# Optimization experiments

Measured on AMD Instinct MI355X. Metric: run time of the kernel, lower is better.

## Reference

```python
import jax, jax.numpy as jnp
import numpy as np
from functools import partial

NUM_HEADS = 6

def _l2norm(x, axis=-1, eps=1e-12):
    n = jnp.sqrt(jnp.sum(x * x, axis=axis, keepdims=True))
    return x / jnp.maximum(n, eps)

def setup_inputs() -> dict:
    key = jax.random.key(0)
    ks = jax.random.split(key, 6)
    b, c, h, w = 2, 192, 256, 256
    x = jax.random.normal(ks[0], (b, c, h, w), dtype=jnp.float32)
    qkv_w = jax.random.normal(ks[1], (3 * c, c), dtype=jnp.float32) * (1.0 / np.sqrt(c))
    dw_w = jax.random.normal(ks[2], (3 * c, 1, 3, 3), dtype=jnp.float32) * (1.0 / 3.0)
    proj_w = jax.random.normal(ks[3], (c, c), dtype=jnp.float32) * (1.0 / np.sqrt(c))
    temperature = jnp.ones((NUM_HEADS, 1, 1), dtype=jnp.float32)
    attn1 = jnp.full((1,), 0.2, dtype=jnp.float32)
    return {"x": x, "qkv_w": qkv_w, "dw_w": dw_w, "proj_w": proj_w,
            "temperature": temperature, "attn1": attn1}

def reference(x, qkv_w, dw_w, proj_w, temperature, attn1):
    b, c, h, w = x.shape
    heads = NUM_HEADS
    C = c // heads          # per-head channel count; attention length
    N = h * w               # spatial 'feature' dim
    # 1x1 conv dim -> 3*dim
    qkv = jnp.einsum('bchw,oc->bohw', x, qkv_w)
    # 3x3 depthwise conv over all 3*dim channels (groups = 3*dim)
    qkv = jax.lax.conv_general_dilated(
        qkv, dw_w, window_strides=(1, 1), padding='SAME',
        feature_group_count=3 * c,
        dimension_numbers=('NCHW', 'OIHW', 'NCHW'))
    q, k, v = jnp.split(qkv, 3, axis=1)
    # b (head C) h w -> b head C (h w)
    q = q.reshape(b, heads, C, N)
    k = k.reshape(b, heads, C, N)
    v = v.reshape(b, heads, C, N)
    q = _l2norm(q)
    k = _l2norm(k)
    # channel attention: [b, head, C, C], tiny matrix
    attn = jnp.einsum('bhcn,bhdn->bhcd', q, k) * temperature[None]
    # top-k (k = C//2) selective mask; kth value threshold == scatter mask
    k1 = C // 2
    kth = jax.lax.top_k(attn, k1)[0][..., -1:]
    attn_m = jnp.where(attn >= kth, attn, -jnp.inf)
    a1 = jax.nn.softmax(attn_m, axis=-1)
    out = jnp.einsum('bhcd,bhdn->bhcn', a1, v)
    # NOTE: original code also computes 2/3, 3/4, 4/5 top-k branches but the
    # returned output uses only out1 * self.attn1 (others are dead code).
    out = out * attn1[0]
    out = out.reshape(b, c, h, w)
    out = jnp.einsum('bchw,oc->bohw', out, proj_w)
    return out
```

## Files before the change

### kernel.cpp

```cpp
#include <hip/hip_runtime.h>
#include <math.h>

#define N_SP 65536
#define IMG  256

typedef __attribute__((ext_vector_type(8))) short s16x8;
typedef __attribute__((ext_vector_type(4))) float f32x4;

__device__ inline ushort f2bf(float f) {
    uint u = __float_as_uint(f);
    return (ushort)((u + 0x7FFFu + ((u >> 16) & 1u)) >> 16);
}
__device__ inline float bf2f(ushort h) { return __uint_as_float(((uint)h) << 16); }
__device__ inline uint pk2(ushort a, ushort b) { return (uint)a | ((uint)b << 16); }

__device__ __forceinline__ void load_lds16(const ushort* g, ushort* l) {
    __builtin_amdgcn_global_load_lds(
        (const __attribute__((address_space(1))) void*)g,
        (__attribute__((address_space(3))) void*)l, 16, 0, 0);
}

__global__ __launch_bounds__(256) void transp_conv(
    const float* __restrict__ src, ushort* __restrict__ hi, ushort* __restrict__ lo)
{
    __shared__ float T[32][65];
    const int t = threadIdx.x;
    const int n0 = blockIdx.x * 64, c0 = blockIdx.y * 32;
    {
        const int cb = t >> 6, n = t & 63;
        #pragma unroll
        for (int i = 0; i < 8; ++i) {
            const int c = cb + i * 4;
            T[c][n] = src[(long long)(c0 + c) * N_SP + n0 + n];
        }
    }
    __syncthreads();
    const int n = t >> 2, cq = (t & 3) * 8;
    float v[8];
    #pragma unroll
    for (int j = 0; j < 8; ++j) v[j] = T[cq + j][n];
    ushort h[8], l[8];
    #pragma unroll
    for (int j = 0; j < 8; ++j) { h[j] = f2bf(v[j]); l[j] = f2bf(v[j] - bf2f(h[j])); }
    uint4 H, L;
    H.x = pk2(h[0], h[1]); H.y = pk2(h[2], h[3]); H.z = pk2(h[4], h[5]); H.w = pk2(h[6], h[7]);
    L.x = pk2(l[0], l[1]); L.y = pk2(l[2], l[3]); L.z = pk2(l[4], l[5]); L.w = pk2(l[6], l[7]);
    const long long o = (long long)(n0 + n) * 192 + c0 + cq;
    *(uint4*)(hi + o) = H;
    *(uint4*)(lo + o) = L;
}

__global__ __launch_bounds__(256) void gemm_mfma(
    const float* __restrict__ Wf, int wrow0,
    const ushort* __restrict__ XtHi, const ushort* __restrict__ XtLo,
    float* __restrict__ C)
{
    __shared__ ushort WsH[64][40], WsL[64][40];
    __shared__ ushort XsH[256 * 32], XsL[256 * 32];
    const int t  = threadIdx.x;
    const int wv = t >> 6, l = t & 63;
    const int lc = l & 15, lg = l >> 4;
    const int m0 = blockIdx.y * 64;
    const long long n0 = (long long)blockIdx.x * 256;

    f32x4 acc[4][4];
    #pragma unroll
    for (int i = 0; i < 4; ++i)
        #pragma unroll
        for (int j = 0; j < 4; ++j) acc[i][j] = (f32x4)(0.f);

    const int ar = t >> 2, ak = (t & 3) * 8;
    const int rX  = wv * 64 + (l >> 2);
    const int koX = (l & 3) * 8;
    ushort* lH = &XsH[(wv * 64) * 32];
    ushort* lL = &XsL[(wv * 64) * 32];

    for (int kc = 0; kc < 192; kc += 32) {
        {
            const ushort* gH = XtHi + (n0 + rX) * 192 + kc + koX;
            const ushort* gL = XtLo + (n0 + rX) * 192 + kc + koX;
            #pragma unroll
            for (int i = 0; i < 4; ++i) {
                load_lds16(gH + i * (16 * 192), lH + i * (16 * 32));
                load_lds16(gL + i * (16 * 192), lL + i * (16 * 32));
            }
        }
        {
            const float* wp = Wf + (long long)(wrow0 + m0 + ar) * 192 + kc + ak;
            const float4 a0 = *(const float4*)wp;
            const float4 a1 = *(const float4*)(wp + 4);
            const float v[8] = {a0.x, a0.y, a0.z, a0.w, a1.x, a1.y, a1.z, a1.w};
            ushort h[8], lo_[8];
            #pragma unroll
            for (int j = 0; j < 8; ++j) { h[j] = f2bf(v[j]); lo_[j] = f2bf(v[j] - bf2f(h[j])); }
            uint4 H, L;
            H.x = pk2(h[0],h[1]); H.y = pk2(h[2],h[3]); H.z = pk2(h[4],h[5]); H.w = pk2(h[6],h[7]);
            L.x = pk2(lo_[0],lo_[1]); L.y = pk2(lo_[2],lo_[3]); L.z = pk2(lo_[4],lo_[5]); L.w = pk2(lo_[6],lo_[7]);
            *(uint4*)&WsH[ar][ak] = H;
            *(uint4*)&WsL[ar][ak] = L;
        }
        __syncthreads();

        s16x8 ah[4], al[4];
        #pragma unroll
        for (int mf = 0; mf < 4; ++mf) {
            ah[mf] = *(const s16x8*)&WsH[mf * 16 + lc][lg * 8];
            al[mf] = *(const s16x8*)&WsL[mf * 16 + lc][lg * 8];
        }
        #pragma unroll
        for (int nf = 0; nf < 4; ++nf) {
            const int nr = wv * 64 + nf * 16 + lc;
            const s16x8 bh = *(const s16x8*)&XsH[nr * 32 + lg * 8];
            const s16x8 bl = *(const s16x8*)&XsL[nr * 32 + lg * 8];
            #pragma unroll
            for (int mf = 0; mf < 4; ++mf) {
                acc[mf][nf] = __builtin_amdgcn_mfma_f32_16x16x32_bf16(ah[mf], bh, acc[mf][nf], 0, 0, 0);
                acc[mf][nf] = __builtin_amdgcn_mfma_f32_16x16x32_bf16(ah[mf], bl, acc[mf][nf], 0, 0, 0);
                acc[mf][nf] = __builtin_amdgcn_mfma_f32_16x16x32_bf16(al[mf], bh, acc[mf][nf], 0, 0, 0);
            }
        }
        __syncthreads();
    }

    #pragma unroll
    for (int mf = 0; mf < 4; ++mf)
        #pragma unroll
        for (int nf = 0; nf < 4; ++nf) {
            const long long nn = n0 + wv * 64 + nf * 16 + lc;
            #pragma unroll
            for (int j = 0; j < 4; ++j)
                C[(long long)(m0 + mf * 16 + lg * 4 + j) * N_SP + nn] = acc[mf][nf][j];
        }
}

__global__ __launch_bounds__(256) void dwconv8(
    const float* __restrict__ src, const float* __restrict__ dww, float* __restrict__ dst)
{
    const int t = threadIdx.x;
    const int s = blockIdx.x * 256 + t;
    const int y = s >> 5;
    const int x8 = (s & 31) * 8;
    const int cg = blockIdx.y;

    const int xl = (x8 == 0) ? 0 : x8 - 4;
    const int xr = (x8 == 248) ? 248 : x8 + 8;

    #pragma unroll
    for (int i = 0; i < 4; ++i) {
        const int c = cg * 4 + i;
        const float* base = src + ((long long)c << 16);
        const float* wp = dww + c * 9;
        float acc[8];
        #pragma unroll
        for (int j = 0; j < 8; ++j) acc[j] = 0.f;
        #pragma unroll
        for (int dy = 0; dy < 3; ++dy) {
            const int yy = y + dy - 1;
            const bool vld = (yy >= 0 && yy < IMG);
            const float* row = base + (vld ? yy : y) * IMG;
            const float w0 = vld ? wp[dy * 3 + 0] : 0.f;
            const float w1 = vld ? wp[dy * 3 + 1] : 0.f;
            const float w2 = vld ? wp[dy * 3 + 2] : 0.f;
            const float4 Lq = *(const float4*)(row + xl);
            const float4 M0 = *(const float4*)(row + x8);
            const float4 M1 = *(const float4*)(row + x8 + 4);
            const float4 Rq = *(const float4*)(row + xr);
            float vv[10];
            vv[0] = (x8 == 0) ? 0.f : Lq.w;
            vv[1] = M0.x; vv[2] = M0.y; vv[3] = M0.z; vv[4] = M0.w;
            vv[5] = M1.x; vv[6] = M1.y; vv[7] = M1.z; vv[8] = M1.w;
            vv[9] = (x8 == 248) ? 0.f : Rq.x;
            #pragma unroll
            for (int j = 0; j < 8; ++j)
                acc[j] = fmaf(w0, vv[j], fmaf(w1, vv[j + 1], fmaf(w2, vv[j + 2], acc[j])));
        }
        float4 o0, o1;
        o0.x = acc[0]; o0.y = acc[1]; o0.z = acc[2]; o0.w = acc[3];
        o1.x = acc[4]; o1.y = acc[5]; o1.z = acc[6]; o1.w = acc[7];
        float* drow = dst + ((long long)c << 16) + y * IMG + x8;
        *(float4*)drow = o0;
        *(float4*)(drow + 4) = o1;
    }
}

__global__ __launch_bounds__(256) void dwconv_vt(
    const float* __restrict__ src, const float* __restrict__ dww,
    ushort* __restrict__ hi, ushort* __restrict__ lo)
{
    const int t = threadIdx.x;
    const int y  = blockIdx.x;
    const int cg = blockIdx.y;
    const int pxg = t & 31, chq = t >> 5;
    const int x8 = pxg * 8;
    const int c0 = cg * 32 + chq * 4;

    const int xl = (x8 == 0) ? 0 : x8 - 4;
    const int xr = (x8 == 248) ? 248 : x8 + 8;

    float accA[4][8];
    #pragma unroll
    for (int i = 0; i < 4; ++i) {
        const int c = c0 + i;
        const float* base = src + ((long long)c << 16);
        const float* wp = dww + c * 9;
        #pragma unroll
        for (int j = 0; j < 8; ++j) accA[i][j] = 0.f;
        #pragma unroll
        for (int dy = 0; dy < 3; ++dy) {
            const int yy = y + dy - 1;
            const bool vld = (yy >= 0 && yy < IMG);
            const float* row = base + (vld ? yy : y) * IMG;
            const float w0 = vld ? wp[dy * 3 + 0] : 0.f;
            const float w1 = vld ? wp[dy * 3 + 1] : 0.f;
            const float w2 = vld ? wp[dy * 3 + 2] : 0.f;
            const float4 Lq = *(const float4*)(row + xl);
            const float4 M0 = *(const float4*)(row + x8);
            const float4 M1 = *(const float4*)(row + x8 + 4);
            const float4 Rq = *(const float4*)(row + xr);
            float vv[10];
            vv[0] = (x8 == 0) ? 0.f : Lq.w;
            vv[1] = M0.x; vv[2] = M0.y; vv[3] = M0.z; vv[4] = M0.w;
            vv[5] = M1.x; vv[6] = M1.y; vv[7] = M1.z; vv[8] = M1.w;
            vv[9] = (x8 == 248) ? 0.f : Rq.x;
            #pragma unroll
            for (int j = 0; j < 8; ++j)
                accA[i][j] = fmaf(w0, vv[j], fmaf(w1, vv[j + 1], fmaf(w2, vv[j + 2], accA[i][j])));
        }
    }
    const long long nbase = (long long)y * 256 + x8;
    #pragma unroll
    for (int j = 0; j < 8; ++j) {
        ushort h4[4], l4[4];
        #pragma unroll
        for (int i = 0; i < 4; ++i) {
            const float v = accA[i][j];
            h4[i] = f2bf(v);
            l4[i] = f2bf(v - bf2f(h4[i]));
        }
        uint2 H, L;
        H.x = pk2(h4[0], h4[1]); H.y = pk2(h4[2], h4[3]);
        L.x = pk2(l4[0], l4[1]); L.y = pk2(l4[2], l4[3]);
        const long long o = (nbase + j) * 192 + c0;
        *(uint2*)(hi + o) = H;
        *(uint2*)(lo + o) = L;
    }
}

__global__ __launch_bounds__(256) void gred(
    const float* __restrict__ q, const float* __restrict__ k, float* __restrict__ Gpart)
{
    __shared__ float smem[8448];
    float* qs = smem;
    float* ks = smem + 4224;
    const int t = threadIdx.x;
    const int blk = blockIdx.x, h = blockIdx.y;
    const int w = t >> 6, l = t & 63;
    const int cqd = l >> 3, dqd = l & 7;

    float acc[4][4];
    #pragma unroll
    for (int i = 0; i < 4; ++i) { acc[i][0]=0.f; acc[i][1]=0.f; acc[i][2]=0.f; acc[i][3]=0.f; }
    float sq[4] = {0.f,0.f,0.f,0.f}, sk[4] = {0.f,0.f,0.f,0.f};

    const float* qh = q + ((long long)(h * 32) << 16);
    const float* kh = k + ((long long)(h * 32) << 16);

    for (int s = 0; s < 4; ++s) {
        const int n0s = blk * 512 + s * 128;
        #pragma unroll
        for (int i = 0; i < 4; ++i) {
            const int f4 = t + i * 256;
            const int ch = f4 >> 5, n4 = (f4 & 31) * 4;
            const long long go = ((long long)ch << 16) + n0s + n4;
            *(float4*)&qs[ch * 132 + n4] = *(const float4*)(qh + go);
            *(float4*)&ks[ch * 132 + n4] = *(const float4*)(kh + go);
        }
        __syncthreads();
        const int nb = w * 32;
        #pragma unroll
        for (int it = 0; it < 8; ++it) {
            const int n = nb + it * 4;
            float4 qa[4], kb[4];
            #pragma unroll
            for (int i = 0; i < 4; ++i) qa[i] = *(const float4*)&qs[(cqd * 4 + i) * 132 + n];
            #pragma unroll
            for (int j = 0; j < 4; ++j) kb[j] = *(const float4*)&ks[(dqd * 4 + j) * 132 + n];
            #pragma unroll
            for (int i = 0; i < 4; ++i) {
                #pragma unroll
                for (int j = 0; j < 4; ++j) {
                    acc[i][j] = fmaf(qa[i].x, kb[j].x, acc[i][j]);
                    acc[i][j] = fmaf(qa[i].y, kb[j].y, acc[i][j]);
                    acc[i][j] = fmaf(qa[i].z, kb[j].z, acc[i][j]);
                    acc[i][j] = fmaf(qa[i].w, kb[j].w, acc[i][j]);
                }
            }
            if (dqd == 0) {
                #pragma unroll
                for (int i = 0; i < 4; ++i) {
                    sq[i] = fmaf(qa[i].x, qa[i].x, sq[i]);
                    sq[i] = fmaf(qa[i].y, qa[i].y, sq[i]);
                    sq[i] = fmaf(qa[i].z, qa[i].z, sq[i]);
                    sq[i] = fmaf(qa[i].w, qa[i].w, sq[i]);
                }
            }
            if (cqd == 0) {
                #pragma unroll
                for (int j = 0; j < 4; ++j) {
                    sk[j] = fmaf(kb[j].x, kb[j].x, sk[j]);
                    sk[j] = fmaf(kb[j].y, kb[j].y, sk[j]);
                    sk[j] = fmaf(kb[j].z, kb[j].z, sk[j]);
                    sk[j] = fmaf(kb[j].w, kb[j].w, sk[j]);
                }
            }
        }
        __syncthreads();
    }

    float* red  = smem;
    float* red2 = smem + 4096;
    #pragma unroll
    for (int i = 0; i < 4; ++i) {
        #pragma unroll
        for (int j = 0; j < 4; ++j)
            red[w * 1024 + (cqd * 4 + i) * 32 + dqd * 4 + j] = acc[i][j];
    }
    if (dqd == 0) {
        #pragma unroll
        for (int i = 0; i < 4; ++i) red2[w * 32 + cqd * 4 + i] = sq[i];
    }
    if (cqd == 0) {
        #pragma unroll
        for (int j = 0; j < 4; ++j) red2[128 + w * 32 + dqd * 4 + j] = sk[j];
    }
    __syncthreads();

    float* Gp = Gpart + (long long)(h * 128 + blk) * 1088;
    #pragma unroll
    for (int i = 0; i < 4; ++i) {
        int slot = t + i * 256;
        Gp[slot] = red[slot] + red[1024 + slot] + red[2048 + slot] + red[3072 + slot];
    }
    if (t < 32) {
        Gp[1024 + t] = red2[t] + red2[32 + t] + red2[64 + t] + red2[96 + t];
    } else if (t < 64) {
        int c = t - 32;
        Gp[1056 + c] = red2[128 + c] + red2[160 + c] + red2[192 + c] + red2[224 + c];
    }
}

__global__ void reduce_g(const float* __restrict__ Gpart, float* __restrict__ G,
                         float* __restrict__ Sq, float* __restrict__ Sk, int bh0)
{
    const int h = blockIdx.x, t = threadIdx.x;
    const float* Gp = Gpart + (long long)h * 128 * 1088;
    const int bh = bh0 + h;
    #pragma unroll
    for (int i = 0; i < 5; ++i) {
        int slot = t + i * 256;
        if (slot >= 1088) break;
        float s = 0.f;
        for (int tl = 0; tl < 128; ++tl) s += Gp[(long long)tl * 1088 + slot];
        if (slot < 1024)      G[(long long)bh * 1024 + slot] = s;
        else if (slot < 1056) Sq[bh * 32 + (slot - 1024)] = s;
        else                  Sk[bh * 32 + (slot - 1056)] = s;
    }
}

__global__ void attn_small(const float* __restrict__ G, const float* __restrict__ Sq,
                           const float* __restrict__ Sk, const float* __restrict__ temp,
                           const float* __restrict__ attn1, float* __restrict__ A)
{
    const int h = blockIdx.x, b = blockIdx.y, c = threadIdx.x;
    const int bh = b * 6 + h;
    const float* g = G + ((long long)bh * 32 + c) * 32;
    const float nq = fmaxf(sqrtf(Sq[bh * 32 + c]), 1e-12f);
    const float T  = temp[h];
    const float a1 = attn1[0];

    float a[32];
    #pragma unroll
    for (int d = 0; d < 32; ++d) {
        float nk = fmaxf(sqrtf(Sk[bh * 32 + d]), 1e-12f);
        a[d] = g[d] / (nq * nk) * T;
    }
    unsigned mask = 0u;
    float m = 0.f, kth = 0.f;
    for (int it = 0; it < 16; ++it) {
        float best = -3.4e38f; int bi = 0;
        #pragma unroll
        for (int d = 0; d < 32; ++d) {
            bool avail = ((mask >> d) & 1u) == 0u;
            if (avail && a[d] > best) { best = a[d]; bi = d; }
        }
        mask |= (1u << bi);
        if (it == 0) m = best;
        kth = best;
    }
    float denom = 0.f;
    #pragma unroll
    for (int d = 0; d < 32; ++d) if (a[d] >= kth) denom += expf(a[d] - m);
    const float inv = a1 / denom;
    float* Ar = A + ((long long)bh * 32 + c) * 32;
    #pragma unroll
    for (int d = 0; d < 32; ++d) Ar[d] = (a[d] >= kth) ? expf(a[d] - m) * inv : 0.f;
}

__global__ void make_m(const float* __restrict__ proj_w, const float* __restrict__ A,
                       float* __restrict__ M)
{
    const int o = blockIdx.x, b = blockIdx.y, j = threadIdx.x;
    const int hd = j >> 5, d = j & 31;
    const float* pw = proj_w + o * 192 + hd * 32;
    const float* Ah = A + ((long long)(b * 6 + hd) * 32) * 32 + d;
    float s = 0.f;
    #pragma unroll
    for (int cq = 0; cq < 32; ++cq) s = fmaf(pw[cq], Ah[cq * 32], s);
    M[((long long)(b * 192 + o)) * 192 + j] = s;
}

extern "C" void kernel_launch(void* const* d_in, const int* in_sizes, int n_in,
                              void* d_out, int out_size, void* d_ws, size_t ws_size,
                              hipStream_t stream)
{
    const float* x      = (const float*)d_in[0];
    const float* qkv_w  = (const float*)d_in[1];
    const float* dww    = (const float*)d_in[2];
    const float* proj_w = (const float*)d_in[3];
    const float* temp   = (const float*)d_in[4];
    const float* attn1  = (const float*)d_in[5];
    float* out = (float*)d_out;
    float* wsf = (float*)d_ws;

    float* G   = wsf;
    float* Sq  = G + 12288;
    float* Sk  = Sq + 384;
    float* A   = Sk + 384;
    float* Mm  = A + 12288;
    float* buf = Mm + 73728;

    const long long PL = 12582912LL;
    float* W1 = buf;
    float* W2 = buf + PL;
    float* R1 = out;
    float* R2 = out + PL;

    ushort* R1H = (ushort*)R1; ushort* R1L = R1H + PL;
    ushort* W1H = (ushort*)W1; ushort* W1L = W1H + PL;

    transp_conv<<<dim3(1024, 6), 256, 0, stream>>>(x, R1H, R1L);
    gemm_mfma<<<dim3(256, 6), 256, 0, stream>>>(qkv_w, 0, R1H, R1L, buf);
    dwconv8<<<dim3(32, 48), 256, 0, stream>>>(W1, dww, R2);
    dwconv8<<<dim3(32, 48), 256, 0, stream>>>(W2, dww + 192 * 9, W1);
    gred<<<dim3(128, 6), 256, 0, stream>>>(R2, W1, W2);
    reduce_g<<<dim3(6, 1), 256, 0, stream>>>(W2, G, Sq, Sk, 0);

    transp_conv<<<dim3(1024, 6), 256, 0, stream>>>(x + PL, R1H, R1L);
    gemm_mfma<<<dim3(256, 6), 256, 0, stream>>>(qkv_w, 0, R1H, R1L, buf);
    dwconv8<<<dim3(32, 48), 256, 0, stream>>>(W1, dww, R2);
    dwconv8<<<dim3(32, 48), 256, 0, stream>>>(W2, dww + 192 * 9, W1);
    gred<<<dim3(128, 6), 256, 0, stream>>>(R2, W1, W2);
    reduce_g<<<dim3(6, 1), 256, 0, stream>>>(W2, G, Sq, Sk, 6);

    attn_small<<<dim3(6, 2), 32, 0, stream>>>(G, Sq, Sk, temp, attn1, A);
    make_m<<<dim3(192, 2), 192, 0, stream>>>(proj_w, A, Mm);

    gemm_mfma<<<dim3(256, 3), 256, 0, stream>>>(qkv_w, 384, R1H, R1L, W2);
    dwconv_vt<<<dim3(256, 6), 256, 0, stream>>>(W2, dww + 384 * 9, W1H, W1L);
    gemm_mfma<<<dim3(256, 3), 256, 0, stream>>>(Mm + 36864, 0, W1H, W1L, R2);

    transp_conv<<<dim3(1024, 6), 256, 0, stream>>>(x, R1H, R1L);
    gemm_mfma<<<dim3(256, 3), 256, 0, stream>>>(qkv_w, 384, R1H, R1L, W2);
    dwconv_vt<<<dim3(256, 6), 256, 0, stream>>>(W2, dww + 384 * 9, W1H, W1L);
    gemm_mfma<<<dim3(256, 3), 256, 0, stream>>>(Mm, 0, W1H, W1L, R1);
}
```

Before: 656.0 us.

## Double-buffer LDS tiles in MFMA GEMM to overlap loads with compute

Restructures the 1x1-conv GEMM k-loop with double-buffered LDS for both weight and activation tiles. The next k-chunk's global-to-LDS loads and weight fetch are issued before the MFMA work on the current chunk, and it waits only afterwards. This cuts one barrier per iteration and hides load latency. In exchange it doubles LDS use, which may lower occupancy, and it drops the padding on the weight tile rows, which may add bank conflicts.

```diff
diff --git a/kernel.cpp b/kernel.cpp
--- a/kernel.cpp
+++ b/kernel.cpp
@@ -55,8 +55,8 @@
     const ushort* __restrict__ XtHi, const ushort* __restrict__ XtLo,
     float* __restrict__ C)
 {
-    __shared__ ushort WsH[64][40], WsL[64][40];
-    __shared__ ushort XsH[256 * 32], XsL[256 * 32];
+    __shared__ ushort WsH[2][2048], WsL[2][2048];
+    __shared__ ushort XsH[2][8192], XsL[2][8192];
     const int t  = threadIdx.x;
     const int wv = t >> 6, l = t & 63;
     const int lc = l & 15, lg = l >> 4;
@@ -72,54 +72,94 @@
     const int ar = t >> 2, ak = (t & 3) * 8;
     const int rX  = wv * 64 + (l >> 2);
     const int koX = (l & 3) * 8;
-    ushort* lH = &XsH[(wv * 64) * 32];
-    ushort* lL = &XsL[(wv * 64) * 32];
-
-    for (int kc = 0; kc < 192; kc += 32) {
+    const float*  wbase = Wf + (long long)(wrow0 + m0 + ar) * 192 + ak;
+    const ushort* gHb = XtHi + (n0 + rX) * 192 + koX;
+    const ushort* gLb = XtLo + (n0 + rX) * 192 + koX;
+
+    float4 wa, wb;
+
+    wa = *(const float4*)(wbase);
+    wb = *(const float4*)(wbase + 4);
+    {
+        ushort* lH = &XsH[0][(wv * 64) * 32];
+        ushort* lL = &XsL[0][(wv * 64) * 32];
+        #pragma unroll
+        for (int i = 0; i < 4; ++i) {
+            load_lds16(gHb + i * (16 * 192), lH + i * (16 * 32));
+            load_lds16(gLb + i * (16 * 192), lL + i * (16 * 32));
+        }
+    }
+    asm volatile("s_waitcnt vmcnt(0)" ::: "memory");
+    {
+        const float v0=wa.x,v1=wa.y,v2=wa.z,v3=wa.w,v4=wb.x,v5=wb.y,v6=wb.z,v7=wb.w;
+        ushort h0=f2bf(v0),h1=f2bf(v1),h2=f2bf(v2),h3=f2bf(v3),
+               h4=f2bf(v4),h5=f2bf(v5),h6=f2bf(v6),h7=f2bf(v7);
+        uint4 H, L;
+        H.x=pk2(h0,h1); H.y=pk2(h2,h3); H.z=pk2(h4,h5); H.w=pk2(h6,h7);
+        L.x=pk2(f2bf(v0-bf2f(h0)),f2bf(v1-bf2f(h1)));
+        L.y=pk2(f2bf(v2-bf2f(h2)),f2bf(v3-bf2f(h3)));
+        L.z=pk2(f2bf(v4-bf2f(h4)),f2bf(v5-bf2f(h5)));
+        L.w=pk2(f2bf(v6-bf2f(h6)),f2bf(v7-bf2f(h7)));
+        *(uint4*)&WsH[0][ar * 32 + ak] = H;
+        *(uint4*)&WsL[0][ar * 32 + ak] = L;
+    }
+    __syncthreads();
+
+    #pragma unroll
+    for (int ks = 0; ks < 6; ++ks) {
+        const int cur = ks & 1, nxt = cur ^ 1;
+        if (ks < 5) {
+            const int kc = (ks + 1) * 32;
+            wa = *(const float4*)(wbase + kc);
+            wb = *(const float4*)(wbase + kc + 4);
+            ushort* lH = &XsH[nxt][(wv * 64) * 32];
+            ushort* lL = &XsL[nxt][(wv * 64) * 32];
+            #pragma unroll
+            for (int i = 0; i < 4; ++i) {
+                load_lds16(gHb + kc + i * (16 * 192), lH + i * (16 * 32));
+                load_lds16(gLb + kc + i * (16 * 192), lL + i * (16 * 32));
+            }
+            __builtin_amdgcn_sched_barrier(0);
+        }
         {
-            const ushort* gH = XtHi + (n0 + rX) * 192 + kc + koX;
-            const ushort* gL = XtLo + (n0 + rX) * 192 + kc + koX;
-            #pragma unroll
-            for (int i = 0; i < 4; ++i) {
-                load_lds16(gH + i * (16 * 192), lH + i * (16 * 32));
-                load_lds16(gL + i * (16 * 192), lL + i * (16 * 32));
-            }
-        }
-        {
-            const float* wp = Wf + (long long)(wrow0 + m0 + ar) * 192 + kc + ak;
-            const float4 a0 = *(const float4*)wp;
-            const float4 a1 = *(const float4*)(wp + 4);
-            const float v[8] = {a0.x, a0.y, a0.z, a0.w, a1.x, a1.y, a1.z, a1.w};
-            ushort h[8], lo_[8];
-            #pragma unroll
-            for (int j = 0; j < 8; ++j) { h[j] = f2bf(v[j]); lo_[j] = f2bf(v[j] - bf2f(h[j])); }
-            uint4 H, L;
-            H.x = pk2(h[0],h[1]); H.y = pk2(h[2],h[3]); H.z = pk2(h[4],h[5]); H.w = pk2(h[6],h[7]);
-            L.x = pk2(lo_[0],lo_[1]); L.y = pk2(lo_[2],lo_[3]); L.z = pk2(lo_[4],lo_[5]); L.w = pk2(lo_[6],lo_[7]);
-            *(uint4*)&WsH[ar][ak] = H;
-            *(uint4*)&WsL[ar][ak] = L;
-        }
-        __syncthreads();
-
-        s16x8 ah[4], al[4];
-        #pragma unroll
-        for (int mf = 0; mf < 4; ++mf) {
-            ah[mf] = *(const s16x8*)&WsH[mf * 16 + lc][lg * 8];
-            al[mf] = *(const s16x8*)&WsL[mf * 16 + lc][lg * 8];
-        }
-        #pragma unroll
-        for (int nf = 0; nf < 4; ++nf) {
-            const int nr = wv * 64 + nf * 16 + lc;
-            const s16x8 bh = *(const s16x8*)&XsH[nr * 32 + lg * 8];
-            const s16x8 bl = *(const s16x8*)&XsL[nr * 32 + lg * 8];
+            s16x8 ah[4], al[4];
             #pragma unroll
             for (int mf = 0; mf < 4; ++mf) {
-                acc[mf][nf] = __builtin_amdgcn_mfma_f32_16x16x32_bf16(ah[mf], bh, acc[mf][nf], 0, 0, 0);
-                acc[mf][nf] = __builtin_amdgcn_mfma_f32_16x16x32_bf16(ah[mf], bl, acc[mf][nf], 0, 0, 0);
-                acc[mf][nf] = __builtin_amdgcn_mfma_f32_16x16x32_bf16(al[mf], bh, acc[mf][nf], 0, 0, 0);
-            }
-        }
-        __syncthreads();
+                ah[mf] = *(const s16x8*)&WsH[cur][(mf * 16 + lc) * 32 + lg * 8];
+                al[mf] = *(const s16x8*)&WsL[cur][(mf * 16 + lc) * 32 + lg * 8];
+            }
+            #pragma unroll
+            for (int nf = 0; nf < 4; ++nf) {
+                const int nr = wv * 64 + nf * 16 + lc;
+                const s16x8 bh = *(const s16x8*)&XsH[cur][nr * 32 + lg * 8];
+                const s16x8 bl = *(const s16x8*)&XsL[cur][nr * 32 + lg * 8];
+                #pragma unroll
+                for (int mf = 0; mf < 4; ++mf) {
+                    acc[mf][nf] = __builtin_amdgcn_mfma_f32_16x16x32_bf16(ah[mf], bh, acc[mf][nf], 0, 0, 0);
+                    acc[mf][nf] = __builtin_amdgcn_mfma_f32_16x16x32_bf16(ah[mf], bl, acc[mf][nf], 0, 0, 0);
+                    acc[mf][nf] = __builtin_amdgcn_mfma_f32_16x16x32_bf16(al[mf], bh, acc[mf][nf], 0, 0, 0);
+                }
+            }
+        }
+        if (ks < 5) {
+            asm volatile("s_waitcnt vmcnt(0)" ::: "memory");
+            {
+                const float v0=wa.x,v1=wa.y,v2=wa.z,v3=wa.w,v4=wb.x,v5=wb.y,v6=wb.z,v7=wb.w;
+                ushort h0=f2bf(v0),h1=f2bf(v1),h2=f2bf(v2),h3=f2bf(v3),
+                       h4=f2bf(v4),h5=f2bf(v5),h6=f2bf(v6),h7=f2bf(v7);
+                uint4 H, L;
+                H.x=pk2(h0,h1); H.y=pk2(h2,h3); H.z=pk2(h4,h5); H.w=pk2(h6,h7);
+                L.x=pk2(f2bf(v0-bf2f(h0)),f2bf(v1-bf2f(h1)));
+                L.y=pk2(f2bf(v2-bf2f(h2)),f2bf(v3-bf2f(h3)));
+                L.z=pk2(f2bf(v4-bf2f(h4)),f2bf(v5-bf2f(h5)));
+                L.w=pk2(f2bf(v6-bf2f(h6)),f2bf(v7-bf2f(h7)));
+                *(uint4*)&WsH[nxt][ar * 32 + ak] = H;
+                *(uint4*)&WsL[nxt][ar * 32 + ak] = L;
+            }
+            asm volatile("s_waitcnt lgkmcnt(0)" ::: "memory");
+            __builtin_amdgcn_sched_barrier(0);
+            __builtin_amdgcn_s_barrier();
+        }
     }
 
     #pragma unroll
```

Measured after the change: 707.4 us. 1.08x slower.
